# Optimization experiments

Hardware: AMD Instinct MI355X
Metric: run time of the kernel (lower is better)

Reference implementation:

```python
import jax, jax.numpy as jnp
from jax import lax
import numpy as np

BLANK = 0
PAD = 1
LABEL_SMOOTHING = 0.1
CE_SCALE = 1.0
TEMPERATURE = 1.0

B, T, U1, D, V = 8, 128, 33, 512, 4096  # U1 = U + 1


def setup_inputs() -> dict:
    key = jax.random.key(0)
    k0, k1, k2, k3, k4 = jax.random.split(key, 5)
    x = jax.random.normal(k0, (B, T, U1, D), dtype=jnp.float32)
    weight = jax.random.normal(k1, (V, D), dtype=jnp.float32) * 0.02
    bias = jnp.zeros((V,), dtype=jnp.float32)
    src_lengths = jax.random.randint(k2, (B,), T // 2, T + 1, dtype=jnp.int32)
    tgt_lengths = jax.random.randint(k3, (B,), U1 // 2, U1, dtype=jnp.int32)
    targets = jax.random.randint(k4, (B, U1 - 1), 2, V, dtype=jnp.int32)
    pos = jnp.arange(U1 - 1, dtype=jnp.int32)
    targets = jnp.where(pos[None, :] < tgt_lengths[:, None], targets, PAD)
    return {'x': x, 'weight': weight, 'bias': bias, 'targets': targets,
            'src_lengths': src_lengths, 'tgt_lengths': tgt_lengths}


def _rnnt_neglogp(blank_lp, emit_lp, src_lengths, tgt_lengths):
    """RNN-T forward DP. blank_lp: (B,T,U1) log P(blank); emit_lp: (B,T,U) log P(y_u).
    Returns per-utterance negative log-likelihood, shape (B,)."""
    Bn, Tn, U1n = blank_lp.shape
    # alpha at t=0: can only emit labels -> prefix-sum of emit log-probs
    alpha0 = jnp.concatenate(
        [jnp.zeros((Bn, 1), blank_lp.dtype), jnp.cumsum(emit_lp[:, 0, :], axis=1)], axis=1)

    def t_step(alpha_prev, xs):
        blank_prev, emit_t = xs  # (B,U1), (B,U)
        a = alpha_prev + blank_prev  # blank transition from t-1
        def u_step(c, xu):
            a_u, e_prev = xu  # each (B,)
            c = jnp.logaddexp(a_u, c + e_prev)  # emit transition from u-1 at same t
            return c, c
        _, rest = lax.scan(u_step, a[:, 0], (a[:, 1:].T, emit_t.T))  # rest: (U,B)
        alpha_t = jnp.concatenate([a[:, :1], rest.T], axis=1)
        return alpha_t, alpha_t

    xs = (jnp.swapaxes(blank_lp[:, :-1], 0, 1), jnp.swapaxes(emit_lp[:, 1:], 0, 1))
    _, alphas_rest = lax.scan(t_step, alpha0, xs)  # (T-1,B,U1)
    alphas = jnp.concatenate([alpha0[None], alphas_rest], axis=0)  # (T,B,U1)
    bidx = jnp.arange(Bn)
    alpha_last_t = alphas[src_lengths - 1, bidx]  # (B,U1)
    a_fin = jnp.take_along_axis(alpha_last_t, tgt_lengths[:, None], axis=1)[:, 0]
    b_fin = blank_lp[bidx, src_lengths - 1, tgt_lengths]  # final blank emission
    return -(a_fin + b_fin)


def reference(x, weight, bias, targets, src_lengths, tgt_lengths):
    Vn = weight.shape[0]
    # joint logits over full lattice: (B,T,U1,V)
    logits = (jnp.einsum('btud,vd->btuv', x, weight) + bias).astype(jnp.float32)
    lp = jax.nn.log_softmax(logits / TEMPERATURE, axis=-1)
    blank_lp = lp[..., BLANK]  # (B,T,U1)
    emit_lp = jnp.take_along_axis(lp[:, :, :-1, :], targets[:, None, :, None].astype(jnp.int32), axis=3)[..., 0]  # (B,T,U)
    loss_prob = jnp.sum(_rnnt_neglogp(blank_lp, emit_lp, src_lengths, tgt_lengths))
    loss_delay = jnp.zeros((), jnp.float32)  # delay_func == 'zero'
    # label-smoothed CE on last valid encoder frame
    last_h = jnp.take_along_axis(x, (src_lengths - 1)[:, None, None, None], axis=1)[:, 0]  # (B,U1,D)
    last_h = last_h[:, :-1]  # (B,U,D)
    ce_logits = (jnp.einsum('bud,vd->buv', last_h, weight) + bias).astype(jnp.float32)
    lprobs = jax.nn.log_softmax(ce_logits, axis=-1)
    nll = -jnp.take_along_axis(lprobs, targets[..., None], axis=-1)[..., 0]  # (B,U)
    smooth = -jnp.sum(lprobs, axis=-1)
    mask = (targets != PAD).astype(lprobs.dtype)
    eps_i = LABEL_SMOOTHING / (Vn - 1)
    loss_smoothed = jnp.sum(((1.0 - LABEL_SMOOTHING - eps_i) * nll + eps_i * smooth) * mask)
    total = loss_prob + loss_delay + CE_SCALE * loss_smoothed
    return total
```

## Files before the change

### kernel.cpp

```cpp
#include <hip/hip_runtime.h>
#include <math.h>
#include <stdint.h>

#define B_ 8
#define T_ 128
#define U1_ 33
#define D_ 512
#define V_ 4096
#define M_ (B_*T_*U1_)

#define BLANK_ 0
#define PAD_ 1

#define TM 64
#define TNH 2048
#define CH 128
#define NCH (TNH/CH)
#define BKB 128

#define SCALE_A 0x7F7F7F7Fu
#define SCALE_B 0x79797979u

typedef __attribute__((ext_vector_type(4))) float fvec4;
typedef __attribute__((ext_vector_type(8))) int   i8v;
typedef __attribute__((ext_vector_type(4))) int   i4v;

__device__ __forceinline__ void load_lds16(const uint8_t* g, uint8_t* l) {
    __builtin_amdgcn_global_load_lds(
        (const __attribute__((address_space(1))) unsigned int*)g,
        (__attribute__((address_space(3))) unsigned int*)l, 16, 0, 0);
}

__device__ __forceinline__ unsigned pack4_fp8(fvec4 v) {
    int r = __builtin_amdgcn_cvt_pk_fp8_f32(v.x, v.y, 0, false);
    r = __builtin_amdgcn_cvt_pk_fp8_f32(v.z, v.w, r, true);
    return (unsigned)r;
}

__global__ void wconvert(const float* __restrict__ w, uint8_t* __restrict__ wf8,
                         float* __restrict__ out)
{
    int i = blockIdx.x * 256 + threadIdx.x;
    if (i == 0) out[0] = 0.0f;
    const int nw = (V_ * D_) / 16;
    for (int j = i; j < nw; j += gridDim.x * 256) {
        const fvec4* p = (const fvec4*)w + (size_t)j * 4;
        fvec4 v0 = p[0]*64.0f, v1 = p[1]*64.0f, v2 = p[2]*64.0f, v3 = p[3]*64.0f;
        uint4 o = { pack4_fp8(v0), pack4_fp8(v1), pack4_fp8(v2), pack4_fp8(v3) };
        ((uint4*)wf8)[j] = o;
    }
}

__global__ __launch_bounds__(256, 2)
void gemm_fused(const float* __restrict__ x, const uint8_t* __restrict__ wf8,
                const float* __restrict__ bias, const int* __restrict__ targets,
                float* __restrict__ partial_e, float* __restrict__ partial_z,
                float* __restrict__ blank_z, float* __restrict__ emit_z)
{
    __shared__ __align__(16) uint8_t Bs[2][CH * BKB];
    __shared__ float ps[TM], pz[TM];
    __shared__ int tgt_s[TM];

    const int tid  = threadIdx.x;
    const int lane = tid & 63;
    const int wid  = tid >> 6;
    const int m0   = blockIdx.x * TM;
    const int half = blockIdx.y;
    const int n0   = half * TNH;

    const int wrow = (wid >> 1) * 32;
    const int wcol = (wid & 1) * 64;
    const int m15  = lane & 15;
    const int quad = lane >> 4;

    const int srow = wid * 32 + (lane >> 3);
    const int schk = (lane & 7) ^ ((lane >> 3) & 7);
    const uint8_t* bgp = wf8 + (size_t)(n0 + srow) * D_ + schk * 16;

    auto stageB = [&](int buf, int st) {
        const int chunk = st >> 2, ks = st & 3;
        const uint8_t* bg = bgp + (size_t)chunk * CH * D_ + ks * BKB;
#pragma unroll
        for (int j = 0; j < 4; j++)
            load_lds16(bg + j * 8 * D_, &Bs[buf][(wid * 32 + j * 8) * BKB]);
    };

    if (tid < TM) {
        int row = m0 + tid, u = row % U1_, b = row / (T_ * U1_);
        tgt_s[tid] = (u < U1_ - 1) ? targets[b * (U1_ - 1) + u] : -1;
        ps[tid] = 0.0f; pz[tid] = 0.0f;
    }

    i8v afrag[2][4];
#pragma unroll
    for (int mi = 0; mi < 2; mi++) {
        const float* xr = x + (size_t)(m0 + wrow + mi * 16 + m15) * D_ + quad * 32;
#pragma unroll
        for (int ks = 0; ks < 4; ks++) {
            union { unsigned u[8]; i8v v; } pk;
#pragma unroll
            for (int j = 0; j < 8; j++)
                pk.u[j] = pack4_fp8(*(const fvec4*)(xr + ks * 128 + j * 4));
            afrag[mi][ks] = pk.v;
        }
    }

    fvec4 acc[2][4];
    float se_reg[2][4], sz_reg[2][4];
#pragma unroll
    for (int mi = 0; mi < 2; mi++)
#pragma unroll
        for (int j = 0; j < 4; j++) {
            acc[mi][j] = (fvec4)0.0f;
            se_reg[mi][j] = 0.0f; sz_reg[mi][j] = 0.0f;
        }

    stageB(0, 0);
    __syncthreads();

    const int e   = m15 & 7;
    const int c0b = (((quad << 1) ^ e) << 4);

    for (int chunk = 0; chunk < NCH; chunk++) {
        float bv[4];
#pragma unroll
        for (int ni = 0; ni < 4; ni++)
            bv[ni] = bias[n0 + chunk * CH + wcol + ni * 16 + m15];

#pragma unroll
        for (int ks = 0; ks < 4; ks++) {
            const int cur = ks & 1;
            const int ns = chunk * 4 + ks + 1;
            if (ns < NCH * 4) stageB(cur ^ 1, ns);

            i8v fb[4];
#pragma unroll
            for (int ni = 0; ni < 4; ni++) {
                const int base = (wcol + ni * 16 + m15) * BKB;
                union { i4v h[2]; i8v w; } u;
                u.h[0] = *(const i4v*)&Bs[cur][base + c0b];
                u.h[1] = *(const i4v*)&Bs[cur][base + (c0b ^ 16)];
                fb[ni] = u.w;
            }
#pragma unroll
            for (int mi = 0; mi < 2; mi++)
#pragma unroll
                for (int ni = 0; ni < 4; ni++)
                    acc[mi][ni] = __builtin_amdgcn_mfma_scale_f32_16x16x128_f8f6f4(
                                      afrag[mi][ks], fb[ni], acc[mi][ni],
                                      0, 0, 0, SCALE_A, 0, SCALE_B);
            __syncthreads();
        }

        const int cb = n0 + chunk * CH + wcol + m15;
        const bool bl = (half == 0) && (chunk == 0) && (wcol == 0) && (m15 == 0);
#pragma unroll
        for (int mi = 0; mi < 2; mi++) {
#pragma unroll
            for (int r = 0; r < 4; r++) {
                const int lrow = wrow + mi * 16 + quad * 4 + r;
                const int trg = tgt_s[lrow];
#pragma unroll
                for (int ni = 0; ni < 4; ni++) {
                    float z = acc[mi][ni][r] + bv[ni];
                    se_reg[mi][r] += __expf(z);
                    sz_reg[mi][r] += z;
                    if (trg == cb + ni * 16) emit_z[m0 + lrow] = z;
                }
                if (bl) blank_z[m0 + lrow] = acc[mi][0][r] + bv[0];
            }
        }
#pragma unroll
        for (int mi = 0; mi < 2; mi++)
#pragma unroll
            for (int ni = 0; ni < 4; ni++) acc[mi][ni] = (fvec4)0.0f;
    }

#pragma unroll
    for (int mi = 0; mi < 2; mi++)
#pragma unroll
        for (int r = 0; r < 4; r++) {
            float se = se_reg[mi][r], sz = sz_reg[mi][r];
#pragma unroll
            for (int off = 1; off < 16; off <<= 1) {
                se += __shfl_xor(se, off, 64);
                sz += __shfl_xor(sz, off, 64);
            }
            if (m15 == 0) {
                int lrow = wrow + mi * 16 + quad * 4 + r;
                atomicAdd(&ps[lrow], se);
                atomicAdd(&pz[lrow], sz);
            }
        }
    __syncthreads();
    if (tid < TM) {
        partial_e[(size_t)half * M_ + m0 + tid] = ps[tid];
        partial_z[(size_t)half * M_ + m0 + tid] = pz[tid];
    }
}

__global__ __launch_bounds__(256)
void dp_kernel(const float* __restrict__ pe, const float* __restrict__ pz,
               const float* __restrict__ blank_z, const float* __restrict__ emit_z,
               const int* __restrict__ targets, const int* __restrict__ src_lengths,
               const int* __restrict__ tgt_lengths, float* __restrict__ out)
{
    __shared__ float blp[T_ * U1_];
    __shared__ float elp[T_ * U1_];
    const int tid = threadIdx.x;
    const int b = blockIdx.x;
    const int base = b * T_ * U1_;

    for (int i = tid; i < T_ * U1_; i += 256) {
        int g = base + i;
        float l = __logf(pe[g] + pe[M_ + g]);
        blp[i] = blank_z[g] - l;
        elp[i] = emit_z[g] - l;
    }
    __syncthreads();

    const int sl = src_lengths[b], tl = tgt_lengths[b];

    if (tid < 32) {
        int u = tid;
        int tgt = targets[b * (U1_ - 1) + u];
        float contrib = 0.0f;
        int g = base + (sl - 1) * U1_ + u;
        if (tgt != PAD_) {
            float l = __logf(pe[g] + pe[M_ + g]);
            float sz = pz[g] + pz[M_ + g];
            float nll = l - emit_z[g];
            float smooth = (float)V_ * l - sz;
            const float eps_i = 0.1f / (float)(V_ - 1);
            contrib = (1.0f - 0.1f - eps_i) * nll + eps_i * smooth;
        }
#pragma unroll
        for (int off = 1; off < 32; off <<= 1) contrib += __shfl_xor(contrib, off, 32);
        if (u == 0) atomicAdd(out, contrib);
    }
    if (tid >= 64) return;

    const int u = tid;
    const int ua = (u < U1_) ? u : U1_ - 1;
    float val = 0.0f, afin = 0.0f;

    for (int d = 1; d <= (T_ - 1) + (U1_ - 1); d++) {
        int t = d - u;
        int tb = t - 1; tb = tb < 0 ? 0 : (tb > T_ - 1 ? T_ - 1 : tb);
        int tc = t < 0 ? 0 : (t > T_ - 1 ? T_ - 1 : t);
        float blv = blp[tb * U1_ + ua];
        float elv = elp[tc * U1_ + (ua > 0 ? ua - 1 : 0)];
        float up = __shfl_up(val, 1, 64);
        bool valid = (u < U1_) && (t >= 0) && (t < T_);
        if (valid) {
            if (t == 0) {
                val = up + elv;
            } else if (u == 0) {
                val = val + blv;
            } else {
                float a1 = val + blv;
                float a2 = up + elv;
                float mx = fmaxf(a1, a2), mn = fminf(a1, a2);
                val = mx + log1pf(__expf(mn - mx));
            }
            if (t == sl - 1 && u == tl) afin = val;
        }
    }
#pragma unroll
    for (int off = 1; off < 64; off <<= 1) afin += __shfl_xor(afin, off, 64);
    if (u == 0) {
        float bfin = blp[(sl - 1) * U1_ + tl];
        atomicAdd(out, -(afin + bfin));
    }
}

extern "C" void kernel_launch(void* const* d_in, const int* in_sizes, int n_in,
                              void* d_out, int out_size, void* d_ws, size_t ws_size,
                              hipStream_t stream)
{
    const float* x           = (const float*)d_in[0];
    const float* w           = (const float*)d_in[1];
    const float* bias        = (const float*)d_in[2];
    const int*   targets     = (const int*)d_in[3];
    const int*   src_lengths = (const int*)d_in[4];
    const int*   tgt_lengths = (const int*)d_in[5];
    float* out = (float*)d_out;

    char* p = (char*)d_ws;
    uint8_t* wf8 = (uint8_t*)p;      p += (size_t)V_ * D_;
    float* partial_e = (float*)p;    p += (size_t)2 * M_ * sizeof(float);
    float* partial_z = (float*)p;    p += (size_t)2 * M_ * sizeof(float);
    float* blank_z   = (float*)p;    p += (size_t)M_ * sizeof(float);
    float* emit_z    = (float*)p;    p += (size_t)M_ * sizeof(float);

    wconvert<<<512, 256, 0, stream>>>(w, wf8, out);
    gemm_fused<<<dim3(M_/TM, 2), 256, 0, stream>>>(x, wf8, bias, targets,
                                                   partial_e, partial_z, blank_z, emit_z);
    dp_kernel<<<B_, 256, 0, stream>>>(partial_e, partial_z, blank_z, emit_z,
                                      targets, src_lengths, tgt_lengths, out);
}
```

Baseline: 406.3 us.

## Stage A tile in LDS and prefetch B through registers

Quantized A rows are now written once into a swizzled LDS tile and read as fragments each k-step, rather than held in registers for the whole kernel. The B operand moves from direct global-to-LDS loads to a register-staged prefetch two stages ahead, with stores into the double buffer. The loop is flattened into a single stage loop. The aim is lower register pressure and better overlap of global loads with MFMA, at the cost of 32KB extra LDS (hurting occupancy at 2 blocks per CU) and extra LDS reads per step.

```diff
diff --git a/kernel.cpp b/kernel.cpp
--- a/kernel.cpp
+++ b/kernel.cpp
@@ -17,6 +17,7 @@
 #define CH 128
 #define NCH (TNH/CH)
 #define BKB 128
+#define NST (NCH*4)
 
 #define SCALE_A 0x7F7F7F7Fu
 #define SCALE_B 0x79797979u
@@ -24,12 +25,6 @@
 typedef __attribute__((ext_vector_type(4))) float fvec4;
 typedef __attribute__((ext_vector_type(8))) int   i8v;
 typedef __attribute__((ext_vector_type(4))) int   i4v;
-
-__device__ __forceinline__ void load_lds16(const uint8_t* g, uint8_t* l) {
-    __builtin_amdgcn_global_load_lds(
-        (const __attribute__((address_space(1))) unsigned int*)g,
-        (__attribute__((address_space(3))) unsigned int*)l, 16, 0, 0);
-}
 
 __device__ __forceinline__ unsigned pack4_fp8(fvec4 v) {
     int r = __builtin_amdgcn_cvt_pk_fp8_f32(v.x, v.y, 0, false);
@@ -57,6 +52,7 @@
                 float* __restrict__ partial_e, float* __restrict__ partial_z,
                 float* __restrict__ blank_z, float* __restrict__ emit_z)
 {
+    __shared__ __align__(16) uint8_t As[TM * D_];
     __shared__ __align__(16) uint8_t Bs[2][CH * BKB];
     __shared__ float ps[TM], pz[TM];
     __shared__ int tgt_s[TM];
@@ -73,37 +69,47 @@
     const int m15  = lane & 15;
     const int quad = lane >> 4;
 
-    const int srow = wid * 32 + (lane >> 3);
-    const int schk = (lane & 7) ^ ((lane >> 3) & 7);
-    const uint8_t* bgp = wf8 + (size_t)(n0 + srow) * D_ + schk * 16;
-
-    auto stageB = [&](int buf, int st) {
+    const int br  = tid >> 1;
+    const int bs0 = (tid & 1) * 4;
+    const int be  = br & 7;
+
+    uint4 breg[4];
+    auto loadB = [&](int st) {
         const int chunk = st >> 2, ks = st & 3;
-        const uint8_t* bg = bgp + (size_t)chunk * CH * D_ + ks * BKB;
+        const uint8_t* g = wf8 + (size_t)(n0 + chunk * CH + br) * D_ + ks * BKB;
 #pragma unroll
         for (int j = 0; j < 4; j++)
-            load_lds16(bg + j * 8 * D_, &Bs[buf][(wid * 32 + j * 8) * BKB]);
+            breg[j] = *(const uint4*)(g + (((bs0 + j) ^ be) << 4));
     };
-
+    auto writeB = [&](int buf) {
+#pragma unroll
+        for (int j = 0; j < 4; j++)
+            *(uint4*)&Bs[buf][br * BKB + ((bs0 + j) << 4)] = breg[j];
+    };
+
+    loadB(0);
+
+    {
+        const int ar = tid >> 2, kb = tid & 3, ae = ar & 7;
+        const float* xr = x + (size_t)(m0 + ar) * D_ + kb * 128;
+        uint8_t* dst = &As[ar * D_ + kb * 128];
+#pragma unroll
+        for (int c = 0; c < 8; c++) {
+            const fvec4* p = (const fvec4*)(xr + c * 16);
+            uint4 o = { pack4_fp8(p[0]), pack4_fp8(p[1]),
+                        pack4_fp8(p[2]), pack4_fp8(p[3]) };
+            *(uint4*)(dst + ((c ^ ae) << 4)) = o;
+        }
+    }
     if (tid < TM) {
         int row = m0 + tid, u = row % U1_, b = row / (T_ * U1_);
         tgt_s[tid] = (u < U1_ - 1) ? targets[b * (U1_ - 1) + u] : -1;
         ps[tid] = 0.0f; pz[tid] = 0.0f;
     }
-
-    i8v afrag[2][4];
-#pragma unroll
-    for (int mi = 0; mi < 2; mi++) {
-        const float* xr = x + (size_t)(m0 + wrow + mi * 16 + m15) * D_ + quad * 32;
-#pragma unroll
-        for (int ks = 0; ks < 4; ks++) {
-            union { unsigned u[8]; i8v v; } pk;
-#pragma unroll
-            for (int j = 0; j < 8; j++)
-                pk.u[j] = pack4_fp8(*(const fvec4*)(xr + ks * 128 + j * 4));
-            afrag[mi][ks] = pk.v;
-        }
-    }
+    __syncthreads();
+    writeB(0);
+    loadB(1);
+    __syncthreads();
 
     fvec4 acc[2][4];
     float se_reg[2][4], sz_reg[2][4];
@@ -115,65 +121,76 @@
             se_reg[mi][j] = 0.0f; sz_reg[mi][j] = 0.0f;
         }
 
-    stageB(0, 0);
-    __syncthreads();
-
     const int e   = m15 & 7;
     const int c0b = (((quad << 1) ^ e) << 4);
 
-    for (int chunk = 0; chunk < NCH; chunk++) {
-        float bv[4];
-#pragma unroll
-        for (int ni = 0; ni < 4; ni++)
-            bv[ni] = bias[n0 + chunk * CH + wcol + ni * 16 + m15];
-
-#pragma unroll
-        for (int ks = 0; ks < 4; ks++) {
-            const int cur = ks & 1;
-            const int ns = chunk * 4 + ks + 1;
-            if (ns < NCH * 4) stageB(cur ^ 1, ns);
-
-            i8v fb[4];
-#pragma unroll
-            for (int ni = 0; ni < 4; ni++) {
-                const int base = (wcol + ni * 16 + m15) * BKB;
-                union { i4v h[2]; i8v w; } u;
-                u.h[0] = *(const i4v*)&Bs[cur][base + c0b];
-                u.h[1] = *(const i4v*)&Bs[cur][base + (c0b ^ 16)];
-                fb[ni] = u.w;
+    float bv[4];
+
+    for (int st = 0; st < NST; st++) {
+        const int cur = st & 1;
+        if (st + 1 < NST) {
+            writeB(cur ^ 1);
+            if (st + 2 < NST) loadB(st + 2);
+        }
+        if ((st & 3) == 0) {
+            const int chunk = st >> 2;
+#pragma unroll
+            for (int ni = 0; ni < 4; ni++)
+                bv[ni] = bias[n0 + chunk * CH + wcol + ni * 16 + m15];
+        }
+
+        const int ks = st & 3;
+        i8v fa[2], fb[4];
+#pragma unroll
+        for (int mi = 0; mi < 2; mi++) {
+            const int base = (wrow + mi * 16 + m15) * D_ + ks * BKB;
+            union { i4v h[2]; i8v w; } u;
+            u.h[0] = *(const i4v*)&As[base + c0b];
+            u.h[1] = *(const i4v*)&As[base + (c0b ^ 16)];
+            fa[mi] = u.w;
+        }
+#pragma unroll
+        for (int ni = 0; ni < 4; ni++) {
+            const int base = (wcol + ni * 16 + m15) * BKB;
+            union { i4v h[2]; i8v w; } u;
+            u.h[0] = *(const i4v*)&Bs[cur][base + c0b];
+            u.h[1] = *(const i4v*)&Bs[cur][base + (c0b ^ 16)];
+            fb[ni] = u.w;
+        }
+#pragma unroll
+        for (int mi = 0; mi < 2; mi++)
+#pragma unroll
+            for (int ni = 0; ni < 4; ni++)
+                acc[mi][ni] = __builtin_amdgcn_mfma_scale_f32_16x16x128_f8f6f4(
+                                  fa[mi], fb[ni], acc[mi][ni],
+                                  0, 0, 0, SCALE_A, 0, SCALE_B);
+
+        if ((st & 3) == 3) {
+            const int chunk = st >> 2;
+            const int cb = n0 + chunk * CH + wcol + m15;
+            const bool bl = (half == 0) && (chunk == 0) && (wcol == 0) && (m15 == 0);
+#pragma unroll
+            for (int mi = 0; mi < 2; mi++) {
+#pragma unroll
+                for (int r = 0; r < 4; r++) {
+                    const int lrow = wrow + mi * 16 + quad * 4 + r;
+                    const int trg = tgt_s[lrow];
+#pragma unroll
+                    for (int ni = 0; ni < 4; ni++) {
+                        float z = acc[mi][ni][r] + bv[ni];
+                        se_reg[mi][r] += __expf(z);
+                        sz_reg[mi][r] += z;
+                        if (trg == cb + ni * 16) emit_z[m0 + lrow] = z;
+                    }
+                    if (bl) blank_z[m0 + lrow] = acc[mi][0][r] + bv[0];
+                }
             }
 #pragma unroll
             for (int mi = 0; mi < 2; mi++)
 #pragma unroll
-                for (int ni = 0; ni < 4; ni++)
-                    acc[mi][ni] = __builtin_amdgcn_mfma_scale_f32_16x16x128_f8f6f4(
-                                      afrag[mi][ks], fb[ni], acc[mi][ni],
-                                      0, 0, 0, SCALE_A, 0, SCALE_B);
-            __syncthreads();
-        }
-
-        const int cb = n0 + chunk * CH + wcol + m15;
-        const bool bl = (half == 0) && (chunk == 0) && (wcol == 0) && (m15 == 0);
-#pragma unroll
-        for (int mi = 0; mi < 2; mi++) {
-#pragma unroll
-            for (int r = 0; r < 4; r++) {
-                const int lrow = wrow + mi * 16 + quad * 4 + r;
-                const int trg = tgt_s[lrow];
-#pragma unroll
-                for (int ni = 0; ni < 4; ni++) {
-                    float z = acc[mi][ni][r] + bv[ni];
-                    se_reg[mi][r] += __expf(z);
-                    sz_reg[mi][r] += z;
-                    if (trg == cb + ni * 16) emit_z[m0 + lrow] = z;
-                }
-                if (bl) blank_z[m0 + lrow] = acc[mi][0][r] + bv[0];
-            }
-        }
-#pragma unroll
-        for (int mi = 0; mi < 2; mi++)
-#pragma unroll
-            for (int ni = 0; ni < 4; ni++) acc[mi][ni] = (fvec4)0.0f;
+                for (int ni = 0; ni < 4; ni++) acc[mi][ni] = (fvec4)0.0f;
+        }
+        __syncthreads();
     }
 
 #pragma unroll
```

Result: slower. 553.0 us (+36.1%).
